# Optimization experiments

Measured on AMD Instinct MI355X. Metric: run time of the kernel, lower is better.

Reference implementation:

```python
import jax, jax.numpy as jnp
import numpy as np

N_NODES = 100000
N_EDGES = 1280000
D_IN = 64
D_HID = 64


def _sage_conv(x, src, dst, deg, Wl, bl, Wr):
    # gather source-node features per edge, scatter-mean to destination nodes
    msg = x[src]                                            # [E, d]
    agg = jax.ops.segment_sum(msg, dst, num_segments=N_NODES)  # [N, d]
    mean = agg / deg                                        # [N, d]
    # PyG SAGEConv: lin_l(aggregated) + lin_r(root); bias lives in lin_l
    return mean @ Wl.T + bl + x @ Wr.T


def setup_inputs() -> dict:
    key = jax.random.key(0)
    ks = jax.random.split(key, 10)
    x = jax.random.normal(ks[0], (N_NODES, D_IN), dtype=jnp.float32)
    edge_index = jax.random.randint(ks[1], (2, N_EDGES), 0, N_NODES, dtype=jnp.int64)
    s = 1.0 / np.sqrt(D_IN)
    W1l = jax.random.uniform(ks[2], (D_HID, D_IN), jnp.float32, -s, s)
    W1r = jax.random.uniform(ks[3], (D_HID, D_IN), jnp.float32, -s, s)
    b1 = jax.random.uniform(ks[4], (D_HID,), jnp.float32, -s, s)
    s2 = 1.0 / np.sqrt(D_HID)
    W2l = jax.random.uniform(ks[5], (D_HID, D_HID), jnp.float32, -s2, s2)
    W2r = jax.random.uniform(ks[6], (D_HID, D_HID), jnp.float32, -s2, s2)
    b2 = jax.random.uniform(ks[7], (D_HID,), jnp.float32, -s2, s2)
    Wh = jax.random.uniform(ks[8], (1, D_HID), jnp.float32, -s2, s2)
    bh = jax.random.uniform(ks[9], (1,), jnp.float32, -s2, s2)
    return {"x": x, "edge_index": edge_index, "W1l": W1l, "W1r": W1r, "b1": b1,
            "W2l": W2l, "W2r": W2r, "b2": b2, "Wh": Wh, "bh": bh}


def reference(x, edge_index, W1l, W1r, b1, W2l, W2r, b2, Wh, bh):
    src, dst = edge_index[0], edge_index[1]
    # in-degree for mean aggregation (clamped to avoid div-by-zero)
    deg = jax.ops.segment_sum(jnp.ones((N_EDGES,), jnp.float32), dst,
                              num_segments=N_NODES)
    deg = jnp.maximum(deg, 1.0)[:, None]                    # [N, 1]
    h = jax.nn.relu(_sage_conv(x, src, dst, deg, W1l, b1, W1r))
    h = jax.nn.relu(_sage_conv(h, src, dst, deg, W2l, b2, W2r))
    out = (h @ Wh.T + bh)[:, 0]                             # [N]
    return out, h
```

## Files before the change

### kernel.cpp

```cpp
#include <hip/hip_runtime.h>

#define N_NODES 100000
#define N_EDGES 1280000
#define D 64
#define NPAD 102400
#define CAP 48
#define NBUCK 391
#define BUFCAP 4096

typedef __attribute__((ext_vector_type(8))) short bf16x8;
typedef __attribute__((ext_vector_type(4))) float f32x4;

__device__ __forceinline__ unsigned short f2bf(float f) {
    union { float f; unsigned u; } c; c.f = f;
    unsigned u = c.u;
    return (unsigned short)((u + 0x7FFF + ((u >> 16) & 1)) >> 16);
}
__device__ __forceinline__ float bf2f(unsigned short s) {
    union { unsigned u; float f; } c; c.u = ((unsigned)s) << 16;
    return c.f;
}

#define XQ (N_NODES * 16)
__global__ __launch_bounds__(256) void cvt_kernel(
    const float* __restrict__ x,
    const float* __restrict__ W1l, const float* __restrict__ W1r,
    const float* __restrict__ W2l, const float* __restrict__ W2r,
    unsigned short* __restrict__ xb, unsigned short* __restrict__ h1b,
    unsigned short* __restrict__ wb) {
    int i = blockIdx.x * 256 + threadIdx.x;
    if (i < XQ) {
        float4 v = ((const float4*)x)[i];
        ((ushort4*)xb)[i] = make_ushort4(f2bf(v.x), f2bf(v.y), f2bf(v.z), f2bf(v.w));
    } else if (i < XQ + 32) {
        int k = i - XQ;
        if (k < 16) ((ushort4*)xb) [(size_t)N_NODES * 16 + k]        = make_ushort4(0,0,0,0);
        else        ((ushort4*)h1b)[(size_t)N_NODES * 16 + (k - 16)] = make_ushort4(0,0,0,0);
    } else if (i < XQ + 32 + 4096) {
        int wf = i - XQ - 32;
        int m = wf >> 10, k = wf & 1023;
        const float* s = (m == 0) ? W1l : (m == 1) ? W1r : (m == 2) ? W2l : W2r;
        float4 v = ((const float4*)s)[k];
        ((ushort4*)wb)[(size_t)m * 1024 + k] =
            make_ushort4(f2bf(v.x), f2bf(v.y), f2bf(v.z), f2bf(v.w));
    }
}

__global__ __launch_bounds__(512) void binA_kernel(const int* __restrict__ src,
                                                   const int* __restrict__ dst,
                                                   int* __restrict__ btail,
                                                   int* __restrict__ bucketbuf) {
    __shared__ int cntA[392];
    __shared__ int excl[512];
    __shared__ int basep[392];
    __shared__ int   stage_pk[4096];
    __shared__ short stage_bk[4096];

    const int t  = threadIdx.x;
    const int e0 = blockIdx.x * 4096;
    const int cbatch = min(4096, N_EDGES - e0);

    if (t < 392) cntA[t] = 0;
    __syncthreads();

    int mb[8], mr[8], mpk[8];
#pragma unroll
    for (int i = 0; i < 8; ++i) {
        int idx = i * 512 + t;
        mb[i] = -1;
        if (idx < cbatch) {
            int e = e0 + idx;
            int s = src[e], d = dst[e];
            int b = d >> 8;
            mb[i]  = b;
            mpk[i] = (s << 8) | (d & 255);
            mr[i]  = atomicAdd(&cntA[b], 1);
        }
    }
    __syncthreads();

    excl[t] = (t < 392) ? cntA[t] : 0;
    __syncthreads();
    for (int off = 1; off < 512; off <<= 1) {
        int u = (t >= off) ? excl[t - off] : 0;
        __syncthreads();
        excl[t] += u;
        __syncthreads();
    }
    if (t < NBUCK && cntA[t] > 0)
        basep[t] = atomicAdd(&btail[t], cntA[t]);
    __syncthreads();

#pragma unroll
    for (int i = 0; i < 8; ++i) {
        if (mb[i] >= 0) {
            int b = mb[i];
            int p = excl[b] - cntA[b] + mr[i];
            stage_pk[p] = mpk[i];
            stage_bk[p] = (short)b;
        }
    }
    __syncthreads();

#pragma unroll
    for (int i = 0; i < 8; ++i) {
        int idx = i * 512 + t;
        if (idx < cbatch) {
            int b = stage_bk[idx];
            int k = idx - (excl[b] - cntA[b]);
            int g = basep[b] + k;
            if (g < BUFCAP) bucketbuf[b * BUFCAP + g] = stage_pk[idx];
        }
    }
}

__global__ __launch_bounds__(512) void binB_kernel(const int* __restrict__ btail,
                                                   const int* __restrict__ bucketbuf,
                                                   int* __restrict__ csr,
                                                   int* __restrict__ deg) {
    __shared__ int cur[256];
    __shared__ int lcsr[256 * CAP];

    const int t = threadIdx.x;
    const int b = blockIdx.x;

    if (t < 256) cur[t] = 0;
    __syncthreads();

    int c = btail[b];
    if (c > BUFCAP) c = BUFCAP;
    const int* buf = bucketbuf + b * BUFCAP;
    for (int i = t; i < c; i += 512) {
        int pk = buf[i];
        int nl = pk & 255;
        int s  = pk >> 8;
        int r  = atomicAdd(&cur[nl], 1);
        if (r < CAP) lcsr[nl * CAP + r] = s;
    }
    __syncthreads();

    const int base = b * 256;
    for (int i = t; i < 256 * CAP; i += 512)
        csr[(size_t)base * CAP + i] = lcsr[i];
    if (t < 256) deg[base + t] = cur[t];
}

template <int LAYER>
__global__ __launch_bounds__(512) void layer_kernel(
    const int* __restrict__ csr, const int* __restrict__ deg_g,
    const unsigned short* __restrict__ feat_b,
    const unsigned short* __restrict__ wl_b,
    const float* __restrict__ bl,
    const unsigned short* __restrict__ wr_b,
    unsigned short* __restrict__ hout_b,
    float* __restrict__ hout_f,
    const float* __restrict__ Wh, const float* __restrict__ bh,
    float* __restrict__ out)
{
    __shared__ __align__(16) char lds[18432 + 2048];
    unsigned short* sA = (unsigned short*)lds;
    unsigned short* sX = sA + 64 * 72;
    float* sH    = (float*)lds;
    float* spart = (float*)(lds + 18432);

    const int tid = threadIdx.x;
    const int n0  = blockIdx.x * 64;

#pragma unroll
    for (int i = 0; i < 2; ++i) {
        int idx = tid + 512 * i;
        int row = idx >> 4, c4 = idx & 15;
        int n = n0 + row;
        ushort4 x4 = make_ushort4(0, 0, 0, 0);
        if (n < N_NODES) x4 = ((const ushort4*)feat_b)[(size_t)n * 16 + c4];
        *(ushort4*)(sX + row * 72 + c4 * 4) = x4;
    }

    const ushort4* fb = (const ushort4*)feat_b;
    const int l   = tid & 15;
    const int grp = tid >> 4;
#pragma unroll 1
    for (int p = 0; p < 2; ++p) {
        int rloc = p * 32 + grp;
        int n = n0 + rloc;
        int deg = (n < N_NODES) ? deg_g[n] : 0;
        int len = (deg < CAP) ? deg : CAP;
        const int* row = csr + (size_t)n * CAP;
        float ax = 0.f, ay = 0.f, az = 0.f, aw = 0.f;
        for (int cb = 0; cb < len; cb += 16) {
            int idxl = cb + l;
            int id = (idxl < len) ? row[idxl] : N_NODES;
            ushort4 v[16];
#pragma unroll
            for (int i = 0; i < 16; ++i)
                v[i] = fb[(size_t)__shfl(id, i, 16) * 16 + l];
#pragma unroll
            for (int i = 0; i < 16; ++i) {
                ax += bf2f(v[i].x); ay += bf2f(v[i].y);
                az += bf2f(v[i].z); aw += bf2f(v[i].w);
            }
        }
        float inv = 1.0f / fmaxf((float)deg, 1.0f);
        *(ushort4*)(sA + rloc * 72 + l * 4) =
            make_ushort4(f2bf(ax * inv), f2bf(ay * inv), f2bf(az * inv), f2bf(aw * inv));
    }
    __syncthreads();

    const int w8 = tid >> 6;
    const int rt = w8 & 3, ch = w8 >> 2;
    const int l64 = tid & 63;
    const int rowl = l64 & 15, quad = l64 >> 4;

    const unsigned short* ab = sA + (rt * 16 + rowl) * 72 + quad * 8;
    const unsigned short* xb = sX + (rt * 16 + rowl) * 72 + quad * 8;
    bf16x8 am0 = *(const bf16x8*)(ab);
    bf16x8 am1 = *(const bf16x8*)(ab + 32);
    bf16x8 ax0 = *(const bf16x8*)(xb);
    bf16x8 ax1 = *(const bf16x8*)(xb + 32);
    __syncthreads();

    f32x4 acc2[2];
    float bj2[2];
#pragma unroll
    for (int j2 = 0; j2 < 2; ++j2) {
        int jt = ch * 2 + j2;
        const unsigned short* wlp = wl_b + (jt * 16 + rowl) * 64 + quad * 8;
        const unsigned short* wrp = wr_b + (jt * 16 + rowl) * 64 + quad * 8;
        bf16x8 b0 = *(const bf16x8*)(wlp);
        bf16x8 b1 = *(const bf16x8*)(wlp + 32);
        bf16x8 b2 = *(const bf16x8*)(wrp);
        bf16x8 b3 = *(const bf16x8*)(wrp + 32);
        f32x4 a = {0.f, 0.f, 0.f, 0.f};
        a = __builtin_amdgcn_mfma_f32_16x16x32_bf16(am0, b0, a, 0, 0, 0);
        a = __builtin_amdgcn_mfma_f32_16x16x32_bf16(am1, b1, a, 0, 0, 0);
        a = __builtin_amdgcn_mfma_f32_16x16x32_bf16(ax0, b2, a, 0, 0, 0);
        a = __builtin_amdgcn_mfma_f32_16x16x32_bf16(ax1, b3, a, 0, 0, 0);
        acc2[j2] = a;
        bj2[j2] = bl[jt * 16 + rowl];
    }

#pragma unroll
    for (int j2 = 0; j2 < 2; ++j2) {
        int jt = ch * 2 + j2;
#pragma unroll
        for (int r = 0; r < 4; ++r) {
            int node = rt * 16 + quad * 4 + r;
            sH[node * 68 + jt * 16 + rowl] = fmaxf(acc2[j2][r] + bj2[j2], 0.f);
        }
    }
    __syncthreads();

    if (LAYER == 2) {
        int node = tid >> 3, q = tid & 7;
        float p = 0.f;
#pragma unroll
        for (int c = 0; c < 2; ++c) {
            float4 hv = *(const float4*)(sH + node * 68 + q * 8 + c * 4);
            float4 wv = ((const float4*)Wh)[q * 2 + c];
            p += hv.x * wv.x + hv.y * wv.y + hv.z * wv.z + hv.w * wv.w;
        }
        spart[tid] = p;
    }

#pragma unroll
    for (int i = 0; i < 2; ++i) {
        int idx = tid + 512 * i;
        int row = idx >> 4, c4 = idx & 15;
        int n = n0 + row;
        if (n < N_NODES) {
            const float* hp = sH + row * 68 + c4 * 4;
            if (LAYER == 1) {
                ((ushort4*)hout_b)[(size_t)n * 16 + c4] =
                    make_ushort4(f2bf(hp[0]), f2bf(hp[1]), f2bf(hp[2]), f2bf(hp[3]));
            } else {
                ((float4*)hout_f)[(size_t)n * 16 + c4] =
                    make_float4(hp[0], hp[1], hp[2], hp[3]);
            }
        }
    }

    if (LAYER == 2) {
        __syncthreads();
        if (tid < 64) {
            int n = n0 + tid;
            if (n < N_NODES) {
                float s = bh[0];
#pragma unroll
                for (int k = 0; k < 8; ++k) s += spart[tid * 8 + k];
                out[n] = s;
            }
        }
    }
}

extern "C" void kernel_launch(void* const* d_in, const int* in_sizes, int n_in,
                              void* d_out, int out_size, void* d_ws, size_t ws_size,
                              hipStream_t stream) {
    const float* x   = (const float*)d_in[0];
    const int*   ei  = (const int*)d_in[1];
    const int*   src = ei;
    const int*   dst = ei + N_EDGES;
    const float* W1l = (const float*)d_in[2];
    const float* W1r = (const float*)d_in[3];
    const float* b1  = (const float*)d_in[4];
    const float* W2l = (const float*)d_in[5];
    const float* W2r = (const float*)d_in[6];
    const float* b2  = (const float*)d_in[7];
    const float* Wh  = (const float*)d_in[8];
    const float* bh  = (const float*)d_in[9];

    float* out   = (float*)d_out;
    float* h_out = out + N_NODES;

    int* wsi   = (int*)d_ws;
    int* btail = wsi;
    int* deg   = wsi + 512;
    int* csr   = deg + NPAD;
    unsigned short* wb  = (unsigned short*)(csr + NBUCK * 256 * CAP);
    unsigned short* x_b = wb + 16384;
    unsigned short* h1b = x_b + (size_t)(N_NODES + 1) * D;
    int* bucketbuf = (int*)h1b;

    unsigned short* w1l_b = wb;
    unsigned short* w1r_b = wb + 4096;
    unsigned short* w2l_b = wb + 8192;
    unsigned short* w2r_b = wb + 12288;

    const int AB  = (N_EDGES + 4095) / 4096;
    const int CB  = (XQ + 32 + 4096 + 255) / 256;
    const int DB  = (N_NODES + 63) / 64;

    hipMemsetAsync(btail, 0, 512 * sizeof(int), stream);

    cvt_kernel<<<CB, 256, 0, stream>>>(x, W1l, W1r, W2l, W2r, x_b, h1b, wb);

    binA_kernel<<<AB, 512, 0, stream>>>(src, dst, btail, bucketbuf);
    binB_kernel<<<NBUCK, 512, 0, stream>>>(btail, bucketbuf, csr, deg);

    layer_kernel<1><<<DB, 512, 0, stream>>>(
        csr, deg, x_b, w1l_b, b1, w1r_b, h1b, nullptr, nullptr, nullptr, nullptr);
    layer_kernel<2><<<DB, 512, 0, stream>>>(
        csr, deg, h1b, w2l_b, b2, w2r_b, nullptr, h_out, Wh, bh, out);
}
```

Before: 205.2 us.

## Make layer kernels persistent with atomic tile queue and 8-lane bf16x8 gathers

The layer kernels become persistent: 2048 blocks of 256 threads pull 32-node tiles from an atomic counter instead of launching one 512-thread block per 64 nodes. The neighbor gather now uses 8 lanes per node, each loading 16-byte bf16x8 vectors, so each thread handles one node's row. The aim is better load balance across degree-skewed tiles, higher occupancy through smaller LDS use and launch bounds, and wider memory transactions. In exchange it adds an atomic and an extra barrier per tile. Bounds checks are also dropped, which relies on N_NODES dividing evenly by 32.

```diff
diff --git a/kernel.cpp b/kernel.cpp
--- a/kernel.cpp
+++ b/kernel.cpp
@@ -7,6 +7,8 @@
 #define CAP 48
 #define NBUCK 391
 #define BUFCAP 4096
+#define NTILES 3125
+#define PERSIST 2048
 
 typedef __attribute__((ext_vector_type(8))) short bf16x8;
 typedef __attribute__((ext_vector_type(4))) float f32x4;
@@ -146,7 +148,8 @@
 }
 
 template <int LAYER>
-__global__ __launch_bounds__(512) void layer_kernel(
+__global__ __launch_bounds__(256, 8) void layer_kernel(
+    int* __restrict__ ctr,
     const int* __restrict__ csr, const int* __restrict__ deg_g,
     const unsigned short* __restrict__ feat_b,
     const unsigned short* __restrict__ wl_b,
@@ -157,137 +160,139 @@
     const float* __restrict__ Wh, const float* __restrict__ bh,
     float* __restrict__ out)
 {
-    __shared__ __align__(16) char lds[18432 + 2048];
+    __shared__ __align__(16) char lds[10240 + 1024 + 16];
     unsigned short* sA = (unsigned short*)lds;
-    unsigned short* sX = sA + 64 * 72;
+    unsigned short* sX = sA + 32 * 80;
     float* sH    = (float*)lds;
-    float* spart = (float*)(lds + 18432);
+    float* spart = (float*)(lds + 10240);
+    int*   s_tile = (int*)(lds + 10240 + 1024);
 
     const int tid = threadIdx.x;
-    const int n0  = blockIdx.x * 64;
-
-#pragma unroll
-    for (int i = 0; i < 2; ++i) {
-        int idx = tid + 512 * i;
-        int row = idx >> 4, c4 = idx & 15;
-        int n = n0 + row;
-        ushort4 x4 = make_ushort4(0, 0, 0, 0);
-        if (n < N_NODES) x4 = ((const ushort4*)feat_b)[(size_t)n * 16 + c4];
-        *(ushort4*)(sX + row * 72 + c4 * 4) = x4;
-    }
-
-    const ushort4* fb = (const ushort4*)feat_b;
-    const int l   = tid & 15;
-    const int grp = tid >> 4;
-#pragma unroll 1
-    for (int p = 0; p < 2; ++p) {
-        int rloc = p * 32 + grp;
-        int n = n0 + rloc;
-        int deg = (n < N_NODES) ? deg_g[n] : 0;
-        int len = (deg < CAP) ? deg : CAP;
+    const bf16x8* fb8 = (const bf16x8*)feat_b;
+
+    for (;;) {
+        if (tid == 0) *s_tile = atomicAdd(ctr, 1);
+        __syncthreads();
+        const int tile = *s_tile;
+        if (tile >= NTILES) return;
+        const int n0 = tile * 32;
+
+#pragma unroll
+        for (int i = 0; i < 2; ++i) {
+            int idx = tid + 256 * i;
+            int row = idx >> 4, c4 = idx & 15;
+            ushort4 x4 = ((const ushort4*)feat_b)[(size_t)(n0 + row) * 16 + c4];
+            *(ushort4*)(sX + row * 80 + c4 * 4) = x4;
+        }
+
+        const int l8  = tid & 7;
+        const int grp = tid >> 3;
+        const int n = n0 + grp;
+        const int deg = deg_g[n];
+        const int len = (deg < CAP) ? deg : CAP;
         const int* row = csr + (size_t)n * CAP;
-        float ax = 0.f, ay = 0.f, az = 0.f, aw = 0.f;
-        for (int cb = 0; cb < len; cb += 16) {
-            int idxl = cb + l;
-            int id = (idxl < len) ? row[idxl] : N_NODES;
-            ushort4 v[16];
-#pragma unroll
-            for (int i = 0; i < 16; ++i)
-                v[i] = fb[(size_t)__shfl(id, i, 16) * 16 + l];
-#pragma unroll
-            for (int i = 0; i < 16; ++i) {
-                ax += bf2f(v[i].x); ay += bf2f(v[i].y);
-                az += bf2f(v[i].z); aw += bf2f(v[i].w);
+        float a[8];
+#pragma unroll
+        for (int e = 0; e < 8; ++e) a[e] = 0.f;
+
+        for (int cb = 0; cb < len; cb += 8) {
+            int id = (cb + l8 < len) ? row[cb + l8] : N_NODES;
+            bf16x8 v[8];
+#pragma unroll
+            for (int i = 0; i < 8; ++i)
+                v[i] = fb8[(size_t)__shfl(id, i, 8) * 8 + l8];
+#pragma unroll
+            for (int i = 0; i < 8; ++i) {
+#pragma unroll
+                for (int e = 0; e < 8; ++e)
+                    a[e] += bf2f((unsigned short)v[i][e]);
             }
         }
         float inv = 1.0f / fmaxf((float)deg, 1.0f);
-        *(ushort4*)(sA + rloc * 72 + l * 4) =
-            make_ushort4(f2bf(ax * inv), f2bf(ay * inv), f2bf(az * inv), f2bf(aw * inv));
-    }
-    __syncthreads();
-
-    const int w8 = tid >> 6;
-    const int rt = w8 & 3, ch = w8 >> 2;
-    const int l64 = tid & 63;
-    const int rowl = l64 & 15, quad = l64 >> 4;
-
-    const unsigned short* ab = sA + (rt * 16 + rowl) * 72 + quad * 8;
-    const unsigned short* xb = sX + (rt * 16 + rowl) * 72 + quad * 8;
-    bf16x8 am0 = *(const bf16x8*)(ab);
-    bf16x8 am1 = *(const bf16x8*)(ab + 32);
-    bf16x8 ax0 = *(const bf16x8*)(xb);
-    bf16x8 ax1 = *(const bf16x8*)(xb + 32);
-    __syncthreads();
-
-    f32x4 acc2[2];
-    float bj2[2];
-#pragma unroll
-    for (int j2 = 0; j2 < 2; ++j2) {
-        int jt = ch * 2 + j2;
-        const unsigned short* wlp = wl_b + (jt * 16 + rowl) * 64 + quad * 8;
-        const unsigned short* wrp = wr_b + (jt * 16 + rowl) * 64 + quad * 8;
-        bf16x8 b0 = *(const bf16x8*)(wlp);
-        bf16x8 b1 = *(const bf16x8*)(wlp + 32);
-        bf16x8 b2 = *(const bf16x8*)(wrp);
-        bf16x8 b3 = *(const bf16x8*)(wrp + 32);
-        f32x4 a = {0.f, 0.f, 0.f, 0.f};
-        a = __builtin_amdgcn_mfma_f32_16x16x32_bf16(am0, b0, a, 0, 0, 0);
-        a = __builtin_amdgcn_mfma_f32_16x16x32_bf16(am1, b1, a, 0, 0, 0);
-        a = __builtin_amdgcn_mfma_f32_16x16x32_bf16(ax0, b2, a, 0, 0, 0);
-        a = __builtin_amdgcn_mfma_f32_16x16x32_bf16(ax1, b3, a, 0, 0, 0);
-        acc2[j2] = a;
-        bj2[j2] = bl[jt * 16 + rowl];
-    }
-
-#pragma unroll
-    for (int j2 = 0; j2 < 2; ++j2) {
-        int jt = ch * 2 + j2;
-#pragma unroll
-        for (int r = 0; r < 4; ++r) {
-            int node = rt * 16 + quad * 4 + r;
-            sH[node * 68 + jt * 16 + rowl] = fmaxf(acc2[j2][r] + bj2[j2], 0.f);
-        }
-    }
-    __syncthreads();
-
-    if (LAYER == 2) {
-        int node = tid >> 3, q = tid & 7;
-        float p = 0.f;
-#pragma unroll
-        for (int c = 0; c < 2; ++c) {
-            float4 hv = *(const float4*)(sH + node * 68 + q * 8 + c * 4);
-            float4 wv = ((const float4*)Wh)[q * 2 + c];
-            p += hv.x * wv.x + hv.y * wv.y + hv.z * wv.z + hv.w * wv.w;
-        }
-        spart[tid] = p;
-    }
-
-#pragma unroll
-    for (int i = 0; i < 2; ++i) {
-        int idx = tid + 512 * i;
-        int row = idx >> 4, c4 = idx & 15;
-        int n = n0 + row;
-        if (n < N_NODES) {
-            const float* hp = sH + row * 68 + c4 * 4;
+        bf16x8 mv;
+#pragma unroll
+        for (int e = 0; e < 8; ++e) mv[e] = (short)f2bf(a[e] * inv);
+        *(bf16x8*)(sA + grp * 80 + l8 * 8) = mv;
+        __syncthreads();
+
+        const int w4 = tid >> 6;
+        const int rt = w4 & 1, ch = w4 >> 1;
+        const int l64 = tid & 63;
+        const int rowl = l64 & 15, quad = l64 >> 4;
+
+        const unsigned short* ab = sA + (rt * 16 + rowl) * 80 + quad * 8;
+        const unsigned short* xb = sX + (rt * 16 + rowl) * 80 + quad * 8;
+        bf16x8 am0 = *(const bf16x8*)(ab);
+        bf16x8 am1 = *(const bf16x8*)(ab + 32);
+        bf16x8 ax0 = *(const bf16x8*)(xb);
+        bf16x8 ax1 = *(const bf16x8*)(xb + 32);
+        __syncthreads();
+
+        f32x4 acc2[2];
+        float bj2[2];
+#pragma unroll
+        for (int j2 = 0; j2 < 2; ++j2) {
+            int jt = ch * 2 + j2;
+            const unsigned short* wlp = wl_b + (jt * 16 + rowl) * 64 + quad * 8;
+            const unsigned short* wrp = wr_b + (jt * 16 + rowl) * 64 + quad * 8;
+            bf16x8 b0 = *(const bf16x8*)(wlp);
+            bf16x8 b1 = *(const bf16x8*)(wlp + 32);
+            bf16x8 b2 = *(const bf16x8*)(wrp);
+            bf16x8 b3 = *(const bf16x8*)(wrp + 32);
+            f32x4 acc = {0.f, 0.f, 0.f, 0.f};
+            acc = __builtin_amdgcn_mfma_f32_16x16x32_bf16(am0, b0, acc, 0, 0, 0);
+            acc = __builtin_amdgcn_mfma_f32_16x16x32_bf16(am1, b1, acc, 0, 0, 0);
+            acc = __builtin_amdgcn_mfma_f32_16x16x32_bf16(ax0, b2, acc, 0, 0, 0);
+            acc = __builtin_amdgcn_mfma_f32_16x16x32_bf16(ax1, b3, acc, 0, 0, 0);
+            acc2[j2] = acc;
+            bj2[j2] = bl[jt * 16 + rowl];
+        }
+
+#pragma unroll
+        for (int j2 = 0; j2 < 2; ++j2) {
+            int jt = ch * 2 + j2;
+#pragma unroll
+            for (int r = 0; r < 4; ++r) {
+                int node = rt * 16 + quad * 4 + r;
+                sH[node * 72 + jt * 16 + rowl] = fmaxf(acc2[j2][r] + bj2[j2], 0.f);
+            }
+        }
+        __syncthreads();
+
+        if (LAYER == 2) {
+            int node = tid >> 3, q = tid & 7;
+            float p = 0.f;
+#pragma unroll
+            for (int c = 0; c < 2; ++c) {
+                float4 hv = *(const float4*)(sH + node * 72 + q * 8 + c * 4);
+                float4 wv = ((const float4*)Wh)[q * 2 + c];
+                p += hv.x * wv.x + hv.y * wv.y + hv.z * wv.z + hv.w * wv.w;
+            }
+            spart[tid] = p;
+        }
+
+#pragma unroll
+        for (int i = 0; i < 2; ++i) {
+            int idx = tid + 256 * i;
+            int row = idx >> 4, c4 = idx & 15;
+            int nn = n0 + row;
+            const float* hp = sH + row * 72 + c4 * 4;
             if (LAYER == 1) {
-                ((ushort4*)hout_b)[(size_t)n * 16 + c4] =
+                ((ushort4*)hout_b)[(size_t)nn * 16 + c4] =
                     make_ushort4(f2bf(hp[0]), f2bf(hp[1]), f2bf(hp[2]), f2bf(hp[3]));
             } else {
-                ((float4*)hout_f)[(size_t)n * 16 + c4] =
+                ((float4*)hout_f)[(size_t)nn * 16 + c4] =
                     make_float4(hp[0], hp[1], hp[2], hp[3]);
             }
         }
-    }
-
-    if (LAYER == 2) {
-        __syncthreads();
-        if (tid < 64) {
-            int n = n0 + tid;
-            if (n < N_NODES) {
+
+        if (LAYER == 2) {
+            __syncthreads();
+            if (tid < 32) {
                 float s = bh[0];
 #pragma unroll
                 for (int k = 0; k < 8; ++k) s += spart[tid * 8 + k];
-                out[n] = s;
+                out[n0 + tid] = s;
             }
         }
     }
@@ -314,7 +319,9 @@
 
     int* wsi   = (int*)d_ws;
     int* btail = wsi;
-    int* deg   = wsi + 512;
+    int* ctr1  = wsi + 512;
+    int* ctr2  = wsi + 513;
+    int* deg   = wsi + 640;
     int* csr   = deg + NPAD;
     unsigned short* wb  = (unsigned short*)(csr + NBUCK * 256 * CAP);
     unsigned short* x_b = wb + 16384;
@@ -328,17 +335,16 @@
 
     const int AB  = (N_EDGES + 4095) / 4096;
     const int CB  = (XQ + 32 + 4096 + 255) / 256;
-    const int DB  = (N_NODES + 63) / 64;
-
-    hipMemsetAsync(btail, 0, 512 * sizeof(int), stream);
+
+    hipMemsetAsync(btail, 0, 640 * sizeof(int), stream);
 
     cvt_kernel<<<CB, 256, 0, stream>>>(x, W1l, W1r, W2l, W2r, x_b, h1b, wb);
 
     binA_kernel<<<AB, 512, 0, stream>>>(src, dst, btail, bucketbuf);
     binB_kernel<<<NBUCK, 512, 0, stream>>>(btail, bucketbuf, csr, deg);
 
-    layer_kernel<1><<<DB, 512, 0, stream>>>(
-        csr, deg, x_b, w1l_b, b1, w1r_b, h1b, nullptr, nullptr, nullptr, nullptr);
-    layer_kernel<2><<<DB, 512, 0, stream>>>(
-        csr, deg, h1b, w2l_b, b2, w2r_b, nullptr, h_out, Wh, bh, out);
-}
+    layer_kernel<1><<<PERSIST, 256, 0, stream>>>(
+        ctr1, csr, deg, x_b, w1l_b, b1, w1r_b, h1b, nullptr, nullptr, nullptr, nullptr);
+    layer_kernel<2><<<PERSIST, 256, 0, stream>>>(
+        ctr2, csr, deg, h1b, w2l_b, b2, w2r_b, nullptr, h_out, Wh, bh, out);
+}
```

After: 274.3 us. 1.34x slower.

## Make layer kernels persistent with atomic tile counter work stealing

Applied to the files above, without the earlier changes.

Turns both SAGE layer kernels into persistent kernels: a fixed grid of blocks repeatedly takes 64-node tiles from a global atomic counter until all tiles are done. The counters are zeroed together with the existing bucket-tail memset. It also adds a launch-bounds occupancy hint of eight blocks per CU. The aim is to cut block launch overhead and balance the uneven degree-dependent gather work, at the cost of one atomic and an extra barrier per tile.

```diff
diff --git a/kernel.cpp b/kernel.cpp
--- a/kernel.cpp
+++ b/kernel.cpp
@@ -7,6 +7,8 @@
 #define CAP 48
 #define NBUCK 391
 #define BUFCAP 4096
+#define NTILES 1563
+#define PERSIST 1024
 
 typedef __attribute__((ext_vector_type(8))) short bf16x8;
 typedef __attribute__((ext_vector_type(4))) float f32x4;
@@ -146,7 +148,8 @@
 }
 
 template <int LAYER>
-__global__ __launch_bounds__(512) void layer_kernel(
+__global__ __launch_bounds__(512, 8) void layer_kernel(
+    int* __restrict__ ctr,
     const int* __restrict__ csr, const int* __restrict__ deg_g,
     const unsigned short* __restrict__ feat_b,
     const unsigned short* __restrict__ wl_b,
@@ -157,137 +160,145 @@
     const float* __restrict__ Wh, const float* __restrict__ bh,
     float* __restrict__ out)
 {
-    __shared__ __align__(16) char lds[18432 + 2048];
+    __shared__ __align__(16) char lds[18432 + 2048 + 16];
     unsigned short* sA = (unsigned short*)lds;
     unsigned short* sX = sA + 64 * 72;
     float* sH    = (float*)lds;
     float* spart = (float*)(lds + 18432);
+    int*   s_tile = (int*)(lds + 18432 + 2048);
 
     const int tid = threadIdx.x;
-    const int n0  = blockIdx.x * 64;
-
-#pragma unroll
-    for (int i = 0; i < 2; ++i) {
-        int idx = tid + 512 * i;
-        int row = idx >> 4, c4 = idx & 15;
-        int n = n0 + row;
-        ushort4 x4 = make_ushort4(0, 0, 0, 0);
-        if (n < N_NODES) x4 = ((const ushort4*)feat_b)[(size_t)n * 16 + c4];
-        *(ushort4*)(sX + row * 72 + c4 * 4) = x4;
-    }
-
     const ushort4* fb = (const ushort4*)feat_b;
     const int l   = tid & 15;
     const int grp = tid >> 4;
+
+    for (;;) {
+        if (tid == 0) *s_tile = atomicAdd(ctr, 1);
+        __syncthreads();
+        const int tile = *s_tile;
+        if (tile >= NTILES) return;
+        const int n0 = tile * 64;
+
+#pragma unroll
+        for (int i = 0; i < 2; ++i) {
+            int idx = tid + 512 * i;
+            int row = idx >> 4, c4 = idx & 15;
+            int n = n0 + row;
+            ushort4 x4 = make_ushort4(0, 0, 0, 0);
+            if (n < N_NODES) x4 = ((const ushort4*)feat_b)[(size_t)n * 16 + c4];
+            *(ushort4*)(sX + row * 72 + c4 * 4) = x4;
+        }
+
 #pragma unroll 1
-    for (int p = 0; p < 2; ++p) {
-        int rloc = p * 32 + grp;
-        int n = n0 + rloc;
-        int deg = (n < N_NODES) ? deg_g[n] : 0;
-        int len = (deg < CAP) ? deg : CAP;
-        const int* row = csr + (size_t)n * CAP;
-        float ax = 0.f, ay = 0.f, az = 0.f, aw = 0.f;
-        for (int cb = 0; cb < len; cb += 16) {
-            int idxl = cb + l;
-            int id = (idxl < len) ? row[idxl] : N_NODES;
-            ushort4 v[16];
-#pragma unroll
-            for (int i = 0; i < 16; ++i)
-                v[i] = fb[(size_t)__shfl(id, i, 16) * 16 + l];
-#pragma unroll
-            for (int i = 0; i < 16; ++i) {
-                ax += bf2f(v[i].x); ay += bf2f(v[i].y);
-                az += bf2f(v[i].z); aw += bf2f(v[i].w);
-            }
-        }
-        float inv = 1.0f / fmaxf((float)deg, 1.0f);
-        *(ushort4*)(sA + rloc * 72 + l * 4) =
-            make_ushort4(f2bf(ax * inv), f2bf(ay * inv), f2bf(az * inv), f2bf(aw * inv));
-    }
-    __syncthreads();
-
-    const int w8 = tid >> 6;
-    const int rt = w8 & 3, ch = w8 >> 2;
-    const int l64 = tid & 63;
-    const int rowl = l64 & 15, quad = l64 >> 4;
-
-    const unsigned short* ab = sA + (rt * 16 + rowl) * 72 + quad * 8;
-    const unsigned short* xb = sX + (rt * 16 + rowl) * 72 + quad * 8;
-    bf16x8 am0 = *(const bf16x8*)(ab);
-    bf16x8 am1 = *(const bf16x8*)(ab + 32);
-    bf16x8 ax0 = *(const bf16x8*)(xb);
-    bf16x8 ax1 = *(const bf16x8*)(xb + 32);
-    __syncthreads();
-
-    f32x4 acc2[2];
-    float bj2[2];
-#pragma unroll
-    for (int j2 = 0; j2 < 2; ++j2) {
-        int jt = ch * 2 + j2;
-        const unsigned short* wlp = wl_b + (jt * 16 + rowl) * 64 + quad * 8;
-        const unsigned short* wrp = wr_b + (jt * 16 + rowl) * 64 + quad * 8;
-        bf16x8 b0 = *(const bf16x8*)(wlp);
-        bf16x8 b1 = *(const bf16x8*)(wlp + 32);
-        bf16x8 b2 = *(const bf16x8*)(wrp);
-        bf16x8 b3 = *(const bf16x8*)(wrp + 32);
-        f32x4 a = {0.f, 0.f, 0.f, 0.f};
-        a = __builtin_amdgcn_mfma_f32_16x16x32_bf16(am0, b0, a, 0, 0, 0);
-        a = __builtin_amdgcn_mfma_f32_16x16x32_bf16(am1, b1, a, 0, 0, 0);
-        a = __builtin_amdgcn_mfma_f32_16x16x32_bf16(ax0, b2, a, 0, 0, 0);
-        a = __builtin_amdgcn_mfma_f32_16x16x32_bf16(ax1, b3, a, 0, 0, 0);
-        acc2[j2] = a;
-        bj2[j2] = bl[jt * 16 + rowl];
-    }
-
-#pragma unroll
-    for (int j2 = 0; j2 < 2; ++j2) {
-        int jt = ch * 2 + j2;
-#pragma unroll
-        for (int r = 0; r < 4; ++r) {
-            int node = rt * 16 + quad * 4 + r;
-            sH[node * 68 + jt * 16 + rowl] = fmaxf(acc2[j2][r] + bj2[j2], 0.f);
-        }
-    }
-    __syncthreads();
-
-    if (LAYER == 2) {
-        int node = tid >> 3, q = tid & 7;
-        float p = 0.f;
-#pragma unroll
-        for (int c = 0; c < 2; ++c) {
-            float4 hv = *(const float4*)(sH + node * 68 + q * 8 + c * 4);
-            float4 wv = ((const float4*)Wh)[q * 2 + c];
-            p += hv.x * wv.x + hv.y * wv.y + hv.z * wv.z + hv.w * wv.w;
-        }
-        spart[tid] = p;
-    }
-
-#pragma unroll
-    for (int i = 0; i < 2; ++i) {
-        int idx = tid + 512 * i;
-        int row = idx >> 4, c4 = idx & 15;
-        int n = n0 + row;
-        if (n < N_NODES) {
-            const float* hp = sH + row * 68 + c4 * 4;
-            if (LAYER == 1) {
-                ((ushort4*)hout_b)[(size_t)n * 16 + c4] =
-                    make_ushort4(f2bf(hp[0]), f2bf(hp[1]), f2bf(hp[2]), f2bf(hp[3]));
-            } else {
-                ((float4*)hout_f)[(size_t)n * 16 + c4] =
-                    make_float4(hp[0], hp[1], hp[2], hp[3]);
-            }
-        }
-    }
-
-    if (LAYER == 2) {
-        __syncthreads();
-        if (tid < 64) {
-            int n = n0 + tid;
+        for (int p = 0; p < 2; ++p) {
+            int rloc = p * 32 + grp;
+            int n = n0 + rloc;
+            int deg = (n < N_NODES) ? deg_g[n] : 0;
+            int len = (deg < CAP) ? deg : CAP;
+            const int* row = csr + (size_t)n * CAP;
+            float ax = 0.f, ay = 0.f, az = 0.f, aw = 0.f;
+            for (int cb = 0; cb < len; cb += 16) {
+                int idxl = cb + l;
+                int id = (idxl < len) ? row[idxl] : N_NODES;
+                ushort4 v[16];
+#pragma unroll
+                for (int i = 0; i < 16; ++i)
+                    v[i] = fb[(size_t)__shfl(id, i, 16) * 16 + l];
+#pragma unroll
+                for (int i = 0; i < 16; ++i) {
+                    ax += bf2f(v[i].x); ay += bf2f(v[i].y);
+                    az += bf2f(v[i].z); aw += bf2f(v[i].w);
+                }
+            }
+            float inv = 1.0f / fmaxf((float)deg, 1.0f);
+            *(ushort4*)(sA + rloc * 72 + l * 4) =
+                make_ushort4(f2bf(ax * inv), f2bf(ay * inv), f2bf(az * inv), f2bf(aw * inv));
+        }
+        __syncthreads();
+
+        const int w8 = tid >> 6;
+        const int rt = w8 & 3, ch = w8 >> 2;
+        const int l64 = tid & 63;
+        const int rowl = l64 & 15, quad = l64 >> 4;
+
+        const unsigned short* ab = sA + (rt * 16 + rowl) * 72 + quad * 8;
+        const unsigned short* xb = sX + (rt * 16 + rowl) * 72 + quad * 8;
+        bf16x8 am0 = *(const bf16x8*)(ab);
+        bf16x8 am1 = *(const bf16x8*)(ab + 32);
+        bf16x8 ax0 = *(const bf16x8*)(xb);
+        bf16x8 ax1 = *(const bf16x8*)(xb + 32);
+        __syncthreads();
+
+        f32x4 acc2[2];
+        float bj2[2];
+#pragma unroll
+        for (int j2 = 0; j2 < 2; ++j2) {
+            int jt = ch * 2 + j2;
+            const unsigned short* wlp = wl_b + (jt * 16 + rowl) * 64 + quad * 8;
+            const unsigned short* wrp = wr_b + (jt * 16 + rowl) * 64 + quad * 8;
+            bf16x8 b0 = *(const bf16x8*)(wlp);
+            bf16x8 b1 = *(const bf16x8*)(wlp + 32);
+            bf16x8 b2 = *(const bf16x8*)(wrp);
+            bf16x8 b3 = *(const bf16x8*)(wrp + 32);
+            f32x4 acc = {0.f, 0.f, 0.f, 0.f};
+            acc = __builtin_amdgcn_mfma_f32_16x16x32_bf16(am0, b0, acc, 0, 0, 0);
+            acc = __builtin_amdgcn_mfma_f32_16x16x32_bf16(am1, b1, acc, 0, 0, 0);
+            acc = __builtin_amdgcn_mfma_f32_16x16x32_bf16(ax0, b2, acc, 0, 0, 0);
+            acc = __builtin_amdgcn_mfma_f32_16x16x32_bf16(ax1, b3, acc, 0, 0, 0);
+            acc2[j2] = acc;
+            bj2[j2] = bl[jt * 16 + rowl];
+        }
+
+#pragma unroll
+        for (int j2 = 0; j2 < 2; ++j2) {
+            int jt = ch * 2 + j2;
+#pragma unroll
+            for (int r = 0; r < 4; ++r) {
+                int node = rt * 16 + quad * 4 + r;
+                sH[node * 68 + jt * 16 + rowl] = fmaxf(acc2[j2][r] + bj2[j2], 0.f);
+            }
+        }
+        __syncthreads();
+
+        if (LAYER == 2) {
+            int node = tid >> 3, q = tid & 7;
+            float p = 0.f;
+#pragma unroll
+            for (int c = 0; c < 2; ++c) {
+                float4 hv = *(const float4*)(sH + node * 68 + q * 8 + c * 4);
+                float4 wv = ((const float4*)Wh)[q * 2 + c];
+                p += hv.x * wv.x + hv.y * wv.y + hv.z * wv.z + hv.w * wv.w;
+            }
+            spart[tid] = p;
+        }
+
+#pragma unroll
+        for (int i = 0; i < 2; ++i) {
+            int idx = tid + 512 * i;
+            int row = idx >> 4, c4 = idx & 15;
+            int n = n0 + row;
             if (n < N_NODES) {
-                float s = bh[0];
-#pragma unroll
-                for (int k = 0; k < 8; ++k) s += spart[tid * 8 + k];
-                out[n] = s;
+                const float* hp = sH + row * 68 + c4 * 4;
+                if (LAYER == 1) {
+                    ((ushort4*)hout_b)[(size_t)n * 16 + c4] =
+                        make_ushort4(f2bf(hp[0]), f2bf(hp[1]), f2bf(hp[2]), f2bf(hp[3]));
+                } else {
+                    ((float4*)hout_f)[(size_t)n * 16 + c4] =
+                        make_float4(hp[0], hp[1], hp[2], hp[3]);
+                }
+            }
+        }
+
+        if (LAYER == 2) {
+            __syncthreads();
+            if (tid < 64) {
+                int n = n0 + tid;
+                if (n < N_NODES) {
+                    float s = bh[0];
+#pragma unroll
+                    for (int k = 0; k < 8; ++k) s += spart[tid * 8 + k];
+                    out[n] = s;
+                }
             }
         }
     }
@@ -314,7 +325,9 @@
 
     int* wsi   = (int*)d_ws;
     int* btail = wsi;
-    int* deg   = wsi + 512;
+    int* ctr1  = wsi + 512;
+    int* ctr2  = wsi + 513;
+    int* deg   = wsi + 640;
     int* csr   = deg + NPAD;
     unsigned short* wb  = (unsigned short*)(csr + NBUCK * 256 * CAP);
     unsigned short* x_b = wb + 16384;
@@ -328,17 +341,16 @@
 
     const int AB  = (N_EDGES + 4095) / 4096;
     const int CB  = (XQ + 32 + 4096 + 255) / 256;
-    const int DB  = (N_NODES + 63) / 64;
-
-    hipMemsetAsync(btail, 0, 512 * sizeof(int), stream);
+
+    hipMemsetAsync(btail, 0, 640 * sizeof(int), stream);
 
     cvt_kernel<<<CB, 256, 0, stream>>>(x, W1l, W1r, W2l, W2r, x_b, h1b, wb);
 
     binA_kernel<<<AB, 512, 0, stream>>>(src, dst, btail, bucketbuf);
     binB_kernel<<<NBUCK, 512, 0, stream>>>(btail, bucketbuf, csr, deg);
 
-    layer_kernel<1><<<DB, 512, 0, stream>>>(
-        csr, deg, x_b, w1l_b, b1, w1r_b, h1b, nullptr, nullptr, nullptr, nullptr);
-    layer_kernel<2><<<DB, 512, 0, stream>>>(
-        csr, deg, h1b, w2l_b, b2, w2r_b, nullptr, h_out, Wh, bh, out);
-}
+    layer_kernel<1><<<PERSIST, 512, 0, stream>>>(
+        ctr1, csr, deg, x_b, w1l_b, b1, w1r_b, h1b, nullptr, nullptr, nullptr, nullptr);
+    layer_kernel<2><<<PERSIST, 512, 0, stream>>>(
+        ctr2, csr, deg, h1b, w2l_b, b2, w2r_b, nullptr, h_out, Wh, bh, out);
+}
```

Measured after the change: 237.3 us. 1.16x slower.

## Fuse conversion and edge binning into one prep kernel; drop global atomics and memset

Applied to the files above, without the earlier changes.

Merges the bf16 conversion kernel and the edge-binning kernel into a single launch, where the first blocks bucket-sort their edge batch locally and write the sorted batch plus per-bucket offsets, and the remaining blocks do the conversion. The second binning stage now finds each bucket's segments across all batches with a prefix scan and a binary search, instead of reading a fixed-capacity per-bucket buffer filled with global atomics. This removes the memset, one kernel launch and the global atomic contention, and also removes the BUFCAP overflow limit. In exchange it adds a per-element binary search and scattered segment reads in binB.

```diff
diff --git a/kernel.cpp b/kernel.cpp
--- a/kernel.cpp
+++ b/kernel.cpp
@@ -6,7 +6,10 @@
 #define NPAD 102400
 #define CAP 48
 #define NBUCK 391
-#define BUFCAP 4096
+#define AB 313
+#define CVB 1024
+#define NTILES 1563
+#define XQ (N_NODES * 16)
 
 typedef __attribute__((ext_vector_type(8))) short bf16x8;
 typedef __attribute__((ext_vector_type(4))) float f32x4;
@@ -21,117 +24,136 @@
     return c.f;
 }
 
-#define XQ (N_NODES * 16)
-__global__ __launch_bounds__(256) void cvt_kernel(
+__global__ __launch_bounds__(512) void prep_kernel(
     const float* __restrict__ x,
+    const int* __restrict__ src, const int* __restrict__ dst,
     const float* __restrict__ W1l, const float* __restrict__ W1r,
     const float* __restrict__ W2l, const float* __restrict__ W2r,
     unsigned short* __restrict__ xb, unsigned short* __restrict__ h1b,
-    unsigned short* __restrict__ wb) {
-    int i = blockIdx.x * 256 + threadIdx.x;
-    if (i < XQ) {
-        float4 v = ((const float4*)x)[i];
-        ((ushort4*)xb)[i] = make_ushort4(f2bf(v.x), f2bf(v.y), f2bf(v.z), f2bf(v.w));
-    } else if (i < XQ + 32) {
-        int k = i - XQ;
-        if (k < 16) ((ushort4*)xb) [(size_t)N_NODES * 16 + k]        = make_ushort4(0,0,0,0);
-        else        ((ushort4*)h1b)[(size_t)N_NODES * 16 + (k - 16)] = make_ushort4(0,0,0,0);
-    } else if (i < XQ + 32 + 4096) {
-        int wf = i - XQ - 32;
-        int m = wf >> 10, k = wf & 1023;
-        const float* s = (m == 0) ? W1l : (m == 1) ? W1r : (m == 2) ? W2l : W2r;
-        float4 v = ((const float4*)s)[k];
-        ((ushort4*)wb)[(size_t)m * 1024 + k] =
-            make_ushort4(f2bf(v.x), f2bf(v.y), f2bf(v.z), f2bf(v.w));
-    }
-}
-
-__global__ __launch_bounds__(512) void binA_kernel(const int* __restrict__ src,
-                                                   const int* __restrict__ dst,
-                                                   int* __restrict__ btail,
-                                                   int* __restrict__ bucketbuf) {
+    unsigned short* __restrict__ wb,
+    int* __restrict__ sorted, int* __restrict__ exclT)
+{
     __shared__ int cntA[392];
     __shared__ int excl[512];
-    __shared__ int basep[392];
-    __shared__ int   stage_pk[4096];
-    __shared__ short stage_bk[4096];
-
-    const int t  = threadIdx.x;
-    const int e0 = blockIdx.x * 4096;
-    const int cbatch = min(4096, N_EDGES - e0);
-
-    if (t < 392) cntA[t] = 0;
-    __syncthreads();
-
-    int mb[8], mr[8], mpk[8];
-#pragma unroll
-    for (int i = 0; i < 8; ++i) {
-        int idx = i * 512 + t;
-        mb[i] = -1;
-        if (idx < cbatch) {
-            int e = e0 + idx;
-            int s = src[e], d = dst[e];
-            int b = d >> 8;
-            mb[i]  = b;
-            mpk[i] = (s << 8) | (d & 255);
-            mr[i]  = atomicAdd(&cntA[b], 1);
-        }
-    }
-    __syncthreads();
-
-    excl[t] = (t < 392) ? cntA[t] : 0;
-    __syncthreads();
-    for (int off = 1; off < 512; off <<= 1) {
-        int u = (t >= off) ? excl[t - off] : 0;
-        __syncthreads();
-        excl[t] += u;
-        __syncthreads();
-    }
-    if (t < NBUCK && cntA[t] > 0)
-        basep[t] = atomicAdd(&btail[t], cntA[t]);
-    __syncthreads();
-
-#pragma unroll
-    for (int i = 0; i < 8; ++i) {
-        if (mb[i] >= 0) {
-            int b = mb[i];
-            int p = excl[b] - cntA[b] + mr[i];
-            stage_pk[p] = mpk[i];
-            stage_bk[p] = (short)b;
-        }
-    }
-    __syncthreads();
-
-#pragma unroll
-    for (int i = 0; i < 8; ++i) {
-        int idx = i * 512 + t;
-        if (idx < cbatch) {
-            int b = stage_bk[idx];
-            int k = idx - (excl[b] - cntA[b]);
-            int g = basep[b] + k;
-            if (g < BUFCAP) bucketbuf[b * BUFCAP + g] = stage_pk[idx];
-        }
-    }
-}
-
-__global__ __launch_bounds__(512) void binB_kernel(const int* __restrict__ btail,
-                                                   const int* __restrict__ bucketbuf,
+    __shared__ int stage_pk[4096];
+
+    const int t   = threadIdx.x;
+    const int bid = blockIdx.x;
+
+    if (bid < AB) {
+        const int e0 = bid * 4096;
+        const int cbatch = min(4096, N_EDGES - e0);
+
+        if (t < 392) cntA[t] = 0;
+        __syncthreads();
+
+        int mb[8], mr[8], mpk[8];
+#pragma unroll
+        for (int i = 0; i < 8; ++i) {
+            int idx = i * 512 + t;
+            mb[i] = -1;
+            if (idx < cbatch) {
+                int e = e0 + idx;
+                int s = src[e], d = dst[e];
+                int b = d >> 8;
+                mb[i]  = b;
+                mpk[i] = (s << 8) | (d & 255);
+                mr[i]  = atomicAdd(&cntA[b], 1);
+            }
+        }
+        __syncthreads();
+
+        excl[t] = (t < 392) ? cntA[t] : 0;
+        __syncthreads();
+        for (int off = 1; off < 512; off <<= 1) {
+            int u = (t >= off) ? excl[t - off] : 0;
+            __syncthreads();
+            excl[t] += u;
+            __syncthreads();
+        }
+
+#pragma unroll
+        for (int i = 0; i < 8; ++i) {
+            if (mb[i] >= 0) {
+                int b = mb[i];
+                stage_pk[excl[b] - cntA[b] + mr[i]] = mpk[i];
+            }
+        }
+        __syncthreads();
+
+#pragma unroll
+        for (int i = 0; i < 8; ++i) {
+            int idx = i * 512 + t;
+            if (idx < cbatch) sorted[e0 + idx] = stage_pk[idx];
+        }
+        if (t < 392) exclT[bid * 392 + t] = excl[t] - cntA[t];
+    } else {
+        const int gtid = (bid - AB) * 512 + t;
+        const int gsz  = CVB * 512;
+        const int TOT  = XQ + 32 + 4096;
+        for (int i = gtid; i < TOT; i += gsz) {
+            if (i < XQ) {
+                float4 v = ((const float4*)x)[i];
+                ((ushort4*)xb)[i] = make_ushort4(f2bf(v.x), f2bf(v.y), f2bf(v.z), f2bf(v.w));
+            } else if (i < XQ + 32) {
+                int k = i - XQ;
+                if (k < 16) ((ushort4*)xb) [(size_t)N_NODES * 16 + k]        = make_ushort4(0,0,0,0);
+                else        ((ushort4*)h1b)[(size_t)N_NODES * 16 + (k - 16)] = make_ushort4(0,0,0,0);
+            } else {
+                int wf = i - XQ - 32;
+                int m = wf >> 10, k = wf & 1023;
+                const float* s = (m == 0) ? W1l : (m == 1) ? W1r : (m == 2) ? W2l : W2r;
+                float4 v = ((const float4*)s)[k];
+                ((ushort4*)wb)[m * 1024 + k] =
+                    make_ushort4(f2bf(v.x), f2bf(v.y), f2bf(v.z), f2bf(v.w));
+            }
+        }
+    }
+}
+
+__global__ __launch_bounds__(512) void binB_kernel(const int* __restrict__ sorted,
+                                                   const int* __restrict__ exclT,
                                                    int* __restrict__ csr,
                                                    int* __restrict__ deg) {
     __shared__ int cur[256];
     __shared__ int lcsr[256 * CAP];
+    __shared__ int scan[512];
+    __shared__ int segstart[314];
+    __shared__ int segsrc[313];
 
     const int t = threadIdx.x;
-    const int b = blockIdx.x;
+    const int k = blockIdx.x;
 
     if (t < 256) cur[t] = 0;
-    __syncthreads();
-
-    int c = btail[b];
-    if (c > BUFCAP) c = BUFCAP;
-    const int* buf = bucketbuf + b * BUFCAP;
-    for (int i = t; i < c; i += 512) {
-        int pk = buf[i];
+
+    int cnt = 0, s0 = 0;
+    if (t < AB) {
+        s0  = exclT[t * 392 + k];
+        cnt = exclT[t * 392 + k + 1] - s0;
+    }
+    scan[t] = (t < AB) ? cnt : 0;
+    __syncthreads();
+    for (int off = 1; off < 512; off <<= 1) {
+        int u = (t >= off) ? scan[t - off] : 0;
+        __syncthreads();
+        scan[t] += u;
+        __syncthreads();
+    }
+    if (t < AB) {
+        segstart[t] = scan[t] - cnt;
+        segsrc[t]   = t * 4096 + s0;
+    }
+    if (t == AB - 1) segstart[AB] = scan[AB - 1];
+    __syncthreads();
+
+    const int Tk = segstart[AB];
+    for (int i = t; i < Tk; i += 512) {
+        int lo = 0, hi = AB;
+        while (hi - lo > 1) {
+            int mid = (lo + hi) >> 1;
+            if (segstart[mid] <= i) lo = mid; else hi = mid;
+        }
+        int pk = sorted[segsrc[lo] + (i - segstart[lo])];
         int nl = pk & 255;
         int s  = pk >> 8;
         int r  = atomicAdd(&cur[nl], 1);
@@ -139,7 +161,7 @@
     }
     __syncthreads();
 
-    const int base = b * 256;
+    const int base = k * 256;
     for (int i = t; i < 256 * CAP; i += 512)
         csr[(size_t)base * CAP + i] = lcsr[i];
     if (t < 256) deg[base + t] = cur[t];
@@ -230,12 +252,12 @@
         bf16x8 b1 = *(const bf16x8*)(wlp + 32);
         bf16x8 b2 = *(const bf16x8*)(wrp);
         bf16x8 b3 = *(const bf16x8*)(wrp + 32);
-        f32x4 a = {0.f, 0.f, 0.f, 0.f};
-        a = __builtin_amdgcn_mfma_f32_16x16x32_bf16(am0, b0, a, 0, 0, 0);
-        a = __builtin_amdgcn_mfma_f32_16x16x32_bf16(am1, b1, a, 0, 0, 0);
-        a = __builtin_amdgcn_mfma_f32_16x16x32_bf16(ax0, b2, a, 0, 0, 0);
-        a = __builtin_amdgcn_mfma_f32_16x16x32_bf16(ax1, b3, a, 0, 0, 0);
-        acc2[j2] = a;
+        f32x4 acc = {0.f, 0.f, 0.f, 0.f};
+        acc = __builtin_amdgcn_mfma_f32_16x16x32_bf16(am0, b0, acc, 0, 0, 0);
+        acc = __builtin_amdgcn_mfma_f32_16x16x32_bf16(am1, b1, acc, 0, 0, 0);
+        acc = __builtin_amdgcn_mfma_f32_16x16x32_bf16(ax0, b2, acc, 0, 0, 0);
+        acc = __builtin_amdgcn_mfma_f32_16x16x32_bf16(ax1, b3, acc, 0, 0, 0);
+        acc2[j2] = acc;
         bj2[j2] = bl[jt * 16 + rowl];
     }
 
@@ -312,33 +334,27 @@
     float* out   = (float*)d_out;
     float* h_out = out + N_NODES;
 
-    int* wsi   = (int*)d_ws;
-    int* btail = wsi;
-    int* deg   = wsi + 512;
-    int* csr   = deg + NPAD;
+    int* wsi = (int*)d_ws;
+    int* deg = wsi;
+    int* csr = deg + NPAD;
     unsigned short* wb  = (unsigned short*)(csr + NBUCK * 256 * CAP);
     unsigned short* x_b = wb + 16384;
     unsigned short* h1b = x_b + (size_t)(N_NODES + 1) * D;
-    int* bucketbuf = (int*)h1b;
+    int* sorted = (int*)h1b;
+    int* exclT  = sorted + AB * 4096;
 
     unsigned short* w1l_b = wb;
     unsigned short* w1r_b = wb + 4096;
     unsigned short* w2l_b = wb + 8192;
     unsigned short* w2r_b = wb + 12288;
 
-    const int AB  = (N_EDGES + 4095) / 4096;
-    const int CB  = (XQ + 32 + 4096 + 255) / 256;
-    const int DB  = (N_NODES + 63) / 64;
-
-    hipMemsetAsync(btail, 0, 512 * sizeof(int), stream);
-
-    cvt_kernel<<<CB, 256, 0, stream>>>(x, W1l, W1r, W2l, W2r, x_b, h1b, wb);
-
-    binA_kernel<<<AB, 512, 0, stream>>>(src, dst, btail, bucketbuf);
-    binB_kernel<<<NBUCK, 512, 0, stream>>>(btail, bucketbuf, csr, deg);
-
-    layer_kernel<1><<<DB, 512, 0, stream>>>(
+    prep_kernel<<<AB + CVB, 512, 0, stream>>>(
+        x, src, dst, W1l, W1r, W2l, W2r, x_b, h1b, wb, sorted, exclT);
+
+    binB_kernel<<<NBUCK, 512, 0, stream>>>(sorted, exclT, csr, deg);
+
+    layer_kernel<1><<<NTILES, 512, 0, stream>>>(
         csr, deg, x_b, w1l_b, b1, w1r_b, h1b, nullptr, nullptr, nullptr, nullptr);
-    layer_kernel<2><<<DB, 512, 0, stream>>>(
+    layer_kernel<2><<<NTILES, 512, 0, stream>>>(
         csr, deg, h1b, w2l_b, b2, w2r_b, nullptr, h_out, Wh, bh, out);
 }
```

New measurement: 196.3 us. -4.3%, faster.
